# Performance work log

Measured on AMD Instinct MI355X. Metric: run time of the kernel, lower is better.

## Reference

```python
import jax, jax.numpy as jnp
import numpy as np

N_NODES = 200000
N_EVENTS = 100000
MEM_DIM = 100
TIME_DIM = 100
MSG_DIM = 172
T_MAX = 1000000


def setup_inputs() -> dict:
    key = jax.random.key(0)
    ks = jax.random.split(key, 12)
    s = 0.05
    return {
        "memory": jax.random.normal(ks[0], (N_NODES, MEM_DIM), jnp.float32),
        "raw_msg": jax.random.normal(ks[1], (N_EVENTS, MSG_DIM), jnp.float32),
        "time_w": jax.random.normal(ks[2], (TIME_DIM, 1), jnp.float32) * s,
        "time_b": jax.random.normal(ks[3], (TIME_DIM,), jnp.float32) * s,
        "w_ih": jax.random.normal(ks[4], (3 * MEM_DIM, 2 * MEM_DIM + MSG_DIM + TIME_DIM), jnp.float32) * s,
        "w_hh": jax.random.normal(ks[5], (3 * MEM_DIM, MEM_DIM), jnp.float32) * s,
        "b_ih": jax.random.normal(ks[6], (3 * MEM_DIM,), jnp.float32) * s,
        "b_hh": jax.random.normal(ks[7], (3 * MEM_DIM,), jnp.float32) * s,
        "last_update": jax.random.randint(ks[8], (N_NODES,), 0, T_MAX, jnp.int32),
        "src": jax.random.randint(ks[9], (N_EVENTS,), 0, N_NODES, jnp.int32),
        "dst": jax.random.randint(ks[10], (N_EVENTS,), 0, N_NODES, jnp.int32),
        "t": jax.random.randint(ks[11], (N_EVENTS,), 0, T_MAX, jnp.int32),
    }


def _time_enc(t_rel, time_w, time_b):
    # Linear(1, time_dim) followed by cos, as in TGN.update_memory
    return jnp.cos(t_rel[:, None] * time_w[:, 0][None, :] + time_b[None, :])


def _gru_cell(x, h, w_ih, w_hh, b_ih, b_hh):
    gi = x @ w_ih.T + b_ih  # [N, 3*D]
    gh = h @ w_hh.T + b_hh
    i_r, i_z, i_n = jnp.split(gi, 3, axis=-1)
    h_r, h_z, h_n = jnp.split(gh, 3, axis=-1)
    r = jax.nn.sigmoid(i_r + h_r)
    z = jax.nn.sigmoid(i_z + h_z)
    n = jnp.tanh(i_n + r * h_n)
    return (1.0 - z) * n + z * h


def reference(memory, raw_msg, time_w, time_b, w_ih, w_hh, b_ih, b_hh,
              last_update, src, dst, t):
    # time-relative encodings for source- and destination-side messages
    t_rel_s = (t - last_update[src]).astype(memory.dtype)
    t_rel_d = (t - last_update[dst]).astype(memory.dtype)
    t_enc_s = _time_enc(t_rel_s, time_w, time_b)  # [E, time_dim]
    t_enc_d = _time_enc(t_rel_d, time_w, time_b)

    mem_s = memory[src]  # [E, D]
    mem_d = memory[dst]

    # IdentityMessage: concat(mem_self, mem_other, raw_msg, t_enc)
    msg_s = jnp.concatenate([mem_s, mem_d, raw_msg, t_enc_s], axis=-1)  # [E, 472]
    msg_d = jnp.concatenate([mem_d, mem_s, raw_msg, t_enc_d], axis=-1)

    idx = jnp.concatenate([src, dst], axis=0)          # [2E]
    msgs = jnp.concatenate([msg_s, msg_d], axis=0)      # [2E, 472]

    n_nodes = memory.shape[0]
    # MeanAggregator: per-node mean of incoming messages
    summed = jax.ops.segment_sum(msgs, idx, num_segments=n_nodes)  # [N, 472]
    counts = jax.ops.segment_sum(jnp.ones((idx.shape[0],), memory.dtype), idx,
                                 num_segments=n_nodes)             # [N]
    aggr = summed / jnp.maximum(counts, 1.0)[:, None]

    # GRU memory update, applied only to nodes that received messages
    h_new = _gru_cell(aggr, memory, w_ih, w_hh, b_ih, b_hh)
    touched = (counts > 0)[:, None]
    return jnp.where(touched, h_new, memory)  # [N, memory_dim]
```

## Files before the change

kernel.cpp:

```cpp
#include <hip/hip_runtime.h>
#include <math.h>

#define NND 200000
#define NEV 100000
#define MD 100
#define TD 100
#define MSGD 172
#define NB 64
#define NFRAG 25
#define KS 15
#define BP_ELEMS (KS * NFRAG * 64 * 8)
#define GLS 74

typedef __attribute__((ext_vector_type(8))) short bf16x8;
typedef __attribute__((ext_vector_type(4))) float f32x4;

__device__ __forceinline__ float fast_sigmoid(float x) {
    return 1.0f / (1.0f + __expf(-x));
}
__device__ __forceinline__ float fast_tanh(float x) {
    return fmaf(2.0f, 1.0f / (1.0f + __expf(-2.0f * x)), -1.0f);
}

__device__ __forceinline__ unsigned short f2bf(float f) {
    union { float f; unsigned int u; } v; v.f = f;
    unsigned int r = (v.u + 0x7FFFu + ((v.u >> 16) & 1u)) >> 16;
    return (unsigned short)r;
}
__device__ __forceinline__ float bf2f(unsigned int h) {
    union { unsigned int u; float f; } v; v.u = h << 16;
    return v.f;
}
__device__ __forceinline__ unsigned int pk(float a, float b) {
    unsigned int r;
    asm("v_cvt_pk_bf16_f32 %0, %1, %2" : "=v"(r) : "v"(a), "v"(b));
    return r;
}

__global__ __launch_bounds__(256) void k_count(
    const int* __restrict__ src, const int* __restrict__ dst, int* __restrict__ cnt)
{
    int e = blockIdx.x * 256 + threadIdx.x;
    if (e >= NEV) return;
    atomicAdd(&cnt[src[e]], 1);
    atomicAdd(&cnt[dst[e]], 1);
}

__global__ __launch_bounds__(256) void k_scan1(
    const int* __restrict__ cnt, int* __restrict__ off, int* __restrict__ tpos,
    int* __restrict__ psum, int* __restrict__ psumT)
{
    __shared__ int s1[256], s2[256];
    int t = threadIdx.x, b = blockIdx.x;
    int i0 = b * 1024 + t * 4;
    int v0 = (i0 + 0 < NND) ? cnt[i0 + 0] : 0;
    int v1 = (i0 + 1 < NND) ? cnt[i0 + 1] : 0;
    int v2 = (i0 + 2 < NND) ? cnt[i0 + 2] : 0;
    int v3 = (i0 + 3 < NND) ? cnt[i0 + 3] : 0;
    int f0 = v0 > 0, f1 = v1 > 0, f2 = v2 > 0, f3 = v3 > 0;
    int tsum = v0 + v1 + v2 + v3;
    int fsum = f0 + f1 + f2 + f3;
    s1[t] = tsum; s2[t] = fsum;
    __syncthreads();
    for (int o = 1; o < 256; o <<= 1) {
        int x1 = (t >= o) ? s1[t - o] : 0;
        int x2 = (t >= o) ? s2[t - o] : 0;
        __syncthreads();
        s1[t] += x1; s2[t] += x2;
        __syncthreads();
    }
    int e1 = s1[t] - tsum;
    int e2 = s2[t] - fsum;
    if (i0 + 0 < NND) { off[i0 + 0] = e1;                 tpos[i0 + 0] = e2; }
    if (i0 + 1 < NND) { off[i0 + 1] = e1 + v0;            tpos[i0 + 1] = e2 + f0; }
    if (i0 + 2 < NND) { off[i0 + 2] = e1 + v0 + v1;       tpos[i0 + 2] = e2 + f0 + f1; }
    if (i0 + 3 < NND) { off[i0 + 3] = e1 + v0 + v1 + v2;  tpos[i0 + 3] = e2 + f0 + f1 + f2; }
    if (t == 255) { psum[b] = s1[255]; psumT[b] = s2[255]; }
}

__global__ __launch_bounds__(256) void k_scan2(
    int* __restrict__ psum, int* __restrict__ psumT, int* __restrict__ ntp, int nblk)
{
    __shared__ int s1[256], s2[256];
    int t = threadIdx.x;
    int v1 = (t < nblk) ? psum[t] : 0;
    int v2 = (t < nblk) ? psumT[t] : 0;
    s1[t] = v1; s2[t] = v2;
    __syncthreads();
    for (int o = 1; o < 256; o <<= 1) {
        int x1 = (t >= o) ? s1[t - o] : 0;
        int x2 = (t >= o) ? s2[t - o] : 0;
        __syncthreads();
        s1[t] += x1; s2[t] += x2;
        __syncthreads();
    }
    if (t < nblk) { psum[t] = s1[t] - v1; psumT[t] = s2[t] - v2; }
    if (t == nblk - 1) ntp[0] = s2[t];
}

__global__ __launch_bounds__(256) void k_scan3(
    int* __restrict__ off, int* __restrict__ tpos,
    const int* __restrict__ psum, const int* __restrict__ psumT, int* __restrict__ cur)
{
    int t = threadIdx.x, b = blockIdx.x;
    int base = psum[b];
    int baseT = psumT[b];
    int i0 = b * 1024 + t * 4;
#pragma unroll
    for (int j = 0; j < 4; ++j) {
        int i = i0 + j;
        if (i < NND) {
            int v = off[i] + base;
            off[i] = v;
            cur[i] = v;
            tpos[i] += baseT;
        }
    }
}

__global__ __launch_bounds__(256) void k_copytouch(
    const float* __restrict__ memory, const int* __restrict__ cnt,
    const int* __restrict__ off, const int* __restrict__ tpos,
    float* __restrict__ out, int4* __restrict__ tinfo)
{
    int idx = blockIdx.x * 256 + threadIdx.x;
    if (idx >= NND * 25) return;
    int node = idx / 25, u = idx - node * 25;
    int c = cnt[node];
    if (c == 0) {
        reinterpret_cast<float4*>(out)[idx] =
            reinterpret_cast<const float4*>(memory)[idx];
    } else if (u == 0) {
        tinfo[tpos[node]] = make_int4(node, c, off[node], 0);
    }
}

__global__ __launch_bounds__(256) void k_place(
    const int* __restrict__ src, const int* __restrict__ dst,
    const int* __restrict__ tarr, const int* __restrict__ last_update,
    int* __restrict__ cur, int4* __restrict__ entries)
{
    int e = blockIdx.x * 256 + threadIdx.x;
    if (e >= NEV) return;
    int s = src[e], d = dst[e], tt = tarr[e];
    int slot = atomicAdd(&cur[s], 1);
    entries[slot] = make_int4(d, e, __float_as_int((float)(tt - last_update[s])), s);
    slot = atomicAdd(&cur[d], 1);
    entries[slot] = make_int4(s, e, __float_as_int((float)(tt - last_update[d])), d);
}

__global__ __launch_bounds__(256) void k_convert(
    const float* __restrict__ w_ih, const float* __restrict__ w_hh,
    const float* __restrict__ memory, const float* __restrict__ raw_msg,
    unsigned short* __restrict__ Bp, uint4* __restrict__ membf,
    uint4* __restrict__ rawbf)
{
    int idx = blockIdx.x * 256 + threadIdx.x;
    if (idx < BP_ELEMS) {
        int e = idx & 7;
        int lane = (idx >> 3) & 63;
        int t = idx >> 9;
        int nf = t % 25;
        int ks = t / 25;
        int col = nf * 16 + (lane & 15);
        int k = ks * 32 + ((lane >> 4) << 3) + e;
        float v = 0.0f;
        if (col < 200) {
            if (k < 472) v = w_ih[col * 472 + k];
            if (k < 100) v += w_hh[col * 100 + k];
        } else if (col < 300) {
            if (k < 472) v = w_ih[col * 472 + k];
        } else {
            if (k < 100) v = w_hh[(col - 100) * 100 + k];
        }
        Bp[idx] = f2bf(v);
        return;
    }
    int j = idx - BP_ELEMS;
    if (j < NND * 13) {
        int node = j / 13, u = j - node * 13;
        const float4* ms = reinterpret_cast<const float4*>(memory + (size_t)node * MD);
        uint4 o = (uint4){0u, 0u, 0u, 0u};
        if (u < 12) {
            float4 x = ms[2 * u], y = ms[2 * u + 1];
            o.x = pk(x.x, x.y); o.y = pk(x.z, x.w);
            o.z = pk(y.x, y.y); o.w = pk(y.z, y.w);
        } else {
            float4 x = ms[24];
            o.x = pk(x.x, x.y); o.y = pk(x.z, x.w);
        }
        membf[j] = o;
        return;
    }
    j -= NND * 13;
    if (j < NEV * 22) {
        int e = j / 22, r = j - e * 22;
        const float4* rs = reinterpret_cast<const float4*>(raw_msg + (size_t)e * MSGD);
        float4 x = rs[2 * r];
        float4 y = (float4){0.f, 0.f, 0.f, 0.f};
        if (2 * r + 1 < 43) y = rs[2 * r + 1];
        uint4 o;
        o.x = pk(x.x, x.y); o.y = pk(x.z, x.w);
        o.z = pk(y.x, y.y); o.w = pk(y.z, y.w);
        rawbf[j] = o;
    }
}

__global__ __launch_bounds__(512, 4) void tgn_gemm(
    const uint4* __restrict__ membf,
    const uint4* __restrict__ rawbf, const int4* __restrict__ entries,
    const float* __restrict__ time_w, const float* __restrict__ time_b,
    const unsigned short* __restrict__ Bp,
    const float* __restrict__ b_ih, const float* __restrict__ b_hh,
    const int* __restrict__ ntp, const int4* __restrict__ tinfo,
    float* __restrict__ out)
{
    __shared__ __align__(16) unsigned short lds[64 * 480];
    __shared__ int node_s[NB], cnt_s[NB], off_s[NB];
    int tid = threadIdx.x;
    int n0 = blockIdx.x * NB;
    int nt = ntp[0];
    if (n0 >= nt) return;

    if (tid < NB) {
        int slot = n0 + tid;
        if (slot < nt) {
            int4 ti = tinfo[slot];
            node_s[tid] = ti.x; cnt_s[tid] = ti.y; off_s[tid] = ti.z;
        } else {
            node_s[tid] = -1; cnt_s[tid] = 0; off_s[tid] = 0;
        }
    }
    __syncthreads();

    int lane = tid & 63;
    int wv = tid >> 6;

    {
        int u = lane;
        bool lOther = (u >= 13 && u <= 24);
        bool lRaw   = (u >= 25 && u <= 45);
        bool lMix   = (u == 12);
        bool lR46   = (u == 46);
        bool lTenc  = (u >= 47 && u <= 58);
        int offA = lOther ? (16 * u - 200) : (16 * u - 400);

        float tw[8], tb[8];
#pragma unroll
        for (int j = 0; j < 8; ++j) { tw[j] = 0.f; tb[j] = 0.f; }
        if (lTenc) {
            int d0 = 8 * u - 372;
            float4 wa = *reinterpret_cast<const float4*>(time_w + d0);
            float4 wb = *reinterpret_cast<const float4*>(time_w + d0 + 4);
            float4 ba = *reinterpret_cast<const float4*>(time_b + d0);
            float4 bb = *reinterpret_cast<const float4*>(time_b + d0 + 4);
            tw[0] = wa.x; tw[1] = wa.y; tw[2] = wa.z; tw[3] = wa.w;
            tw[4] = wb.x; tw[5] = wb.y; tw[6] = wb.z; tw[7] = wb.w;
            tb[0] = ba.x; tb[1] = ba.y; tb[2] = ba.z; tb[3] = ba.w;
            tb[4] = bb.x; tb[5] = bb.y; tb[6] = bb.z; tb[7] = bb.w;
        } else if (lR46) {
            float4 wa = *reinterpret_cast<const float4*>(time_w);
            float4 ba = *reinterpret_cast<const float4*>(time_b);
            tw[4] = wa.x; tw[5] = wa.y; tw[6] = wa.z; tw[7] = wa.w;
            tb[4] = ba.x; tb[5] = ba.y; tb[6] = ba.z; tb[7] = ba.w;
        }

        const char* membc = reinterpret_cast<const char*>(membf);
        const char* rawbc = reinterpret_cast<const char*>(rawbf);

#pragma unroll
        for (int half = 0; half < 2; ++half) {
            int rb = wv * 8 + half * 4;
            int cc[4], oo[4];
#pragma unroll
            for (int r = 0; r < 4; ++r) { cc[r] = cnt_s[rb + r]; oo[r] = off_s[rb + r]; }
            int4 en[4];
#pragma unroll
            for (int r = 0; r < 4; ++r)
                en[r] = (cc[r] > 0) ? entries[oo[r]] : make_int4(0, 0, 0, 0);
            uint4 mreg[4];
#pragma unroll
            for (int r = 0; r < 4; ++r) {
                int nd = node_s[rb + r];
                mreg[r] = (u < 13 && nd >= 0) ? membf[(size_t)nd * 13 + u]
                                              : (uint4){0u, 0u, 0u, 0u};
            }
            uint2 gA[4], gB[4];
#pragma unroll
            for (int r = 0; r < 4; ++r) {
                gA[r] = (uint2){0u, 0u}; gB[r] = (uint2){0u, 0u};
                if (cc[r] > 0) {
                    if (lOther) {
                        const char* p = membc + (size_t)en[r].x * 208 + offA;
                        gA[r] = *reinterpret_cast<const uint2*>(p);
                        gB[r] = *reinterpret_cast<const uint2*>(p + 8);
                    } else if (lMix) {
                        gB[r] = *reinterpret_cast<const uint2*>(membc + (size_t)en[r].x * 208);
                    } else if (lRaw) {
                        const char* p = rawbc + (size_t)en[r].y * 352 + offA;
                        gA[r] = *reinterpret_cast<const uint2*>(p);
                        gB[r] = *reinterpret_cast<const uint2*>(p + 8);
                    } else if (lR46) {
                        gA[r] = *reinterpret_cast<const uint2*>(rawbc + (size_t)en[r].y * 352 + 336);
                    }
                }
            }
#pragma unroll
            for (int r = 0; r < 4; ++r) {
                int c = cc[r];
                uint4 o;
                if (u < 12) {
                    o = mreg[r];
                } else if (c == 1) {
                    if (lMix) {
                        o.x = mreg[r].x; o.y = mreg[r].y; o.z = gB[r].x; o.w = gB[r].y;
                    } else if (lTenc) {
                        float trel = __int_as_float(en[r].z);
                        o.x = pk(__cosf(fmaf(trel, tw[0], tb[0])), __cosf(fmaf(trel, tw[1], tb[1])));
                        o.y = pk(__cosf(fmaf(trel, tw[2], tb[2])), __cosf(fmaf(trel, tw[3], tb[3])));
                        o.z = pk(__cosf(fmaf(trel, tw[4], tb[4])), __cosf(fmaf(trel, tw[5], tb[5])));
                        o.w = pk(__cosf(fmaf(trel, tw[6], tb[6])), __cosf(fmaf(trel, tw[7], tb[7])));
                    } else if (lR46) {
                        float trel = __int_as_float(en[r].z);
                        o.x = gA[r].x; o.y = gA[r].y;
                        o.z = pk(__cosf(fmaf(trel, tw[4], tb[4])), __cosf(fmaf(trel, tw[5], tb[5])));
                        o.w = pk(__cosf(fmaf(trel, tw[6], tb[6])), __cosf(fmaf(trel, tw[7], tb[7])));
                    } else {
                        o.x = gA[r].x; o.y = gA[r].y; o.z = gB[r].x; o.w = gB[r].y;
                    }
                } else {
                    float a0 = bf2f(gA[r].x & 0xffffu), a1 = bf2f(gA[r].x >> 16);
                    float a2 = bf2f(gA[r].y & 0xffffu), a3 = bf2f(gA[r].y >> 16);
                    float a4 = bf2f(gB[r].x & 0xffffu), a5 = bf2f(gB[r].x >> 16);
                    float a6 = bf2f(gB[r].y & 0xffffu), a7 = bf2f(gB[r].y >> 16);
                    if ((lTenc || lR46) && c > 0) {
                        float trel = __int_as_float(en[r].z);
                        if (lTenc) {
                            a0 = __cosf(fmaf(trel, tw[0], tb[0]));
                            a1 = __cosf(fmaf(trel, tw[1], tb[1]));
                            a2 = __cosf(fmaf(trel, tw[2], tb[2]));
                            a3 = __cosf(fmaf(trel, tw[3], tb[3]));
                        }
                        a4 = __cosf(fmaf(trel, tw[4], tb[4]));
                        a5 = __cosf(fmaf(trel, tw[5], tb[5]));
                        a6 = __cosf(fmaf(trel, tw[6], tb[6]));
                        a7 = __cosf(fmaf(trel, tw[7], tb[7]));
                    }
                    int4 e2 = (c > 1) ? entries[oo[r] + 1] : en[r];
                    for (int i = 1; i < c; ++i) {
                        int4 ecur = e2;
                        if (i + 1 < c) e2 = entries[oo[r] + i + 1];
                        uint2 hA = (uint2){0u, 0u}, hB = (uint2){0u, 0u};
                        if (lOther) {
                            const char* p = membc + (size_t)ecur.x * 208 + offA;
                            hA = *reinterpret_cast<const uint2*>(p);
                            hB = *reinterpret_cast<const uint2*>(p + 8);
                        } else if (lMix) {
                            hB = *reinterpret_cast<const uint2*>(membc + (size_t)ecur.x * 208);
                        } else if (lRaw) {
                            const char* p = rawbc + (size_t)ecur.y * 352 + offA;
                            hA = *reinterpret_cast<const uint2*>(p);
                            hB = *reinterpret_cast<const uint2*>(p + 8);
                        } else if (lR46) {
                            hA = *reinterpret_cast<const uint2*>(rawbc + (size_t)ecur.y * 352 + 336);
                        }
                        a0 += bf2f(hA.x & 0xffffu); a1 += bf2f(hA.x >> 16);
                        a2 += bf2f(hA.y & 0xffffu); a3 += bf2f(hA.y >> 16);
                        a4 += bf2f(hB.x & 0xffffu); a5 += bf2f(hB.x >> 16);
                        a6 += bf2f(hB.y & 0xffffu); a7 += bf2f(hB.y >> 16);
                        if (lTenc || lR46) {
                            float trel = __int_as_float(ecur.z);
                            if (lTenc) {
                                a0 += __cosf(fmaf(trel, tw[0], tb[0]));
                                a1 += __cosf(fmaf(trel, tw[1], tb[1]));
                                a2 += __cosf(fmaf(trel, tw[2], tb[2]));
                                a3 += __cosf(fmaf(trel, tw[3], tb[3]));
                            }
                            a4 += __cosf(fmaf(trel, tw[4], tb[4]));
                            a5 += __cosf(fmaf(trel, tw[5], tb[5]));
                            a6 += __cosf(fmaf(trel, tw[6], tb[6]));
                            a7 += __cosf(fmaf(trel, tw[7], tb[7]));
                        }
                    }
                    float ci = 1.0f / fmaxf((float)c, 1.0f);
                    if (u == 12) {
                        o.x = mreg[r].x; o.y = mreg[r].y;
                    } else {
                        o.x = pk(a0 * ci, a1 * ci); o.y = pk(a2 * ci, a3 * ci);
                    }
                    o.z = pk(a4 * ci, a5 * ci);
                    o.w = pk(a6 * ci, a7 * ci);
                }
                if (u < 60) {
                    int nl = rb + r;
                    int byte = (nl * 960 + 16 * u) ^ ((nl & 7) << 4);
                    *reinterpret_cast<uint4*>(reinterpret_cast<char*>(lds) + byte) = o;
                }
            }
        }
    }
    __syncthreads();

    int l15 = lane & 15;
    int kg8 = (lane >> 4) << 3;
    int f0 = (wv == 0) ? 0 : (4 + 3 * (wv - 1));
    int cw = (wv == 0) ? 4 : 3;

    f32x4 acc[4][4];
#pragma unroll
    for (int g = 0; g < 4; ++g)
#pragma unroll
        for (int i = 0; i < 4; ++i) acc[g][i] = (f32x4){0.f, 0.f, 0.f, 0.f};

    const bf16x8* BpB = reinterpret_cast<const bf16x8*>(Bp);
    const char* ldsc = reinterpret_cast<const char*>(lds);

#pragma unroll
    for (int ks = 0; ks < KS; ++ks) {
        int k0 = ks * 32 + kg8;
        const bf16x8* bp = BpB + ((size_t)(ks * NFRAG + f0)) * 64 + lane;
        bf16x8 b[4];
#pragma unroll
        for (int i = 0; i < 4; ++i)
            if (i < cw) b[i] = bp[i * 64];
#pragma unroll
        for (int g = 0; g < 4; ++g) {
            int r = g * 16 + l15;
            int ab = (r * 960 + 2 * k0) ^ ((r & 7) << 4);
            bf16x8 a = *reinterpret_cast<const bf16x8*>(ldsc + ab);
#pragma unroll
            for (int i = 0; i < 4; ++i)
                if (i < cw)
                    acc[g][i] = __builtin_amdgcn_mfma_f32_16x16x32_bf16(a, b[i], acc[g][i], 0, 0, 0);
        }
    }

    float mv[13];
    {
        const char* membc = reinterpret_cast<const char*>(membf);
#pragma unroll
        for (int t = 0; t < 13; ++t) {
            int idx = tid + t * 512;
            mv[t] = 0.f;
            if (idx < NB * MD) {
                int n = idx / MD, j = idx - n * MD;
                int nd = node_s[n];
                if (nd >= 0) {
                    unsigned short h = *reinterpret_cast<const unsigned short*>(
                        membc + (size_t)nd * 208 + 2 * j);
                    mv[t] = bf2f((unsigned int)h);
                }
            }
        }
    }

    __syncthreads();

    unsigned short* Gl = lds;
    int kq = (lane >> 4) << 2;
#pragma unroll
    for (int i = 0; i < 4; ++i) {
        if (i < cw) {
            int col = (f0 + i) * 16 + l15;
            float bias = (col < 200) ? (b_ih[col] + b_hh[col])
                       : (col < 300) ? b_ih[col] : b_hh[col - 100];
#pragma unroll
            for (int g = 0; g < 4; ++g) {
                int node = g * 16 + kq;
#pragma unroll
                for (int rp = 0; rp < 2; ++rp) {
                    *reinterpret_cast<unsigned int*>(&Gl[col * GLS + node + 2 * rp]) =
                        pk(acc[g][i][2 * rp] + bias, acc[g][i][2 * rp + 1] + bias);
                }
            }
        }
    }
    __syncthreads();

#pragma unroll
    for (int t = 0; t < 13; ++t) {
        int idx = tid + t * 512;
        if (idx < NB * MD) {
            int n = idx / MD, j = idx - n * MD;
            int nd = node_s[n];
            if (nd >= 0) {
                float rp = bf2f((unsigned int)Gl[j * GLS + n]);
                float zp = bf2f((unsigned int)Gl[(100 + j) * GLS + n]);
                float inp = bf2f((unsigned int)Gl[(200 + j) * GLS + n]);
                float hnp = bf2f((unsigned int)Gl[(300 + j) * GLS + n]);
                float r = fast_sigmoid(rp);
                float z = fast_sigmoid(zp);
                float nn = fast_tanh(fmaf(r, hnp, inp));
                float h = (1.0f - z) * nn + z * mv[t];
                out[(size_t)nd * MD + j] = h;
            }
        }
    }
}

extern "C" void kernel_launch(void* const* d_in, const int* in_sizes, int n_in,
                              void* d_out, int out_size, void* d_ws, size_t ws_size,
                              hipStream_t stream)
{
    const float* memory      = (const float*)d_in[0];
    const float* raw_msg     = (const float*)d_in[1];
    const float* time_w      = (const float*)d_in[2];
    const float* time_b      = (const float*)d_in[3];
    const float* w_ih        = (const float*)d_in[4];
    const float* w_hh        = (const float*)d_in[5];
    const float* b_ih        = (const float*)d_in[6];
    const float* b_hh        = (const float*)d_in[7];
    const int*   last_update = (const int*)d_in[8];
    const int*   src         = (const int*)d_in[9];
    const int*   dst         = (const int*)d_in[10];
    const int*   tarr        = (const int*)d_in[11];
    float* out = (float*)d_out;

    int* cnt   = (int*)d_ws;
    int* off   = cnt + NND;
    int* cur   = off + NND;
    int* tpos  = cur + NND;
    int* psum  = tpos + NND;
    int* psumT = psum + 256;
    int* ntp   = psumT + 256;
    int4* entries = (int4*)(ntp + 4);
    int4* tinfo = entries + 2 * NEV;
    uint4* membf = (uint4*)(tinfo + NND);
    uint4* rawbf = membf + (size_t)NND * 13;
    unsigned short* Bp = (unsigned short*)(rawbf + (size_t)NEV * 22);
    size_t need = (size_t)((char*)(Bp + BP_ELEMS) - (char*)d_ws);
    if (ws_size < need) return;

    const int NBLK = (NND + 1023) / 1024;
    const int NTILE = NND / NB;
    const int CVT_TOTAL = BP_ELEMS + NND * 13 + NEV * 22;

    hipMemsetAsync(cnt, 0, NND * sizeof(int), stream);
    k_convert<<<(CVT_TOTAL + 255) / 256, 256, 0, stream>>>(w_ih, w_hh, memory, raw_msg,
                                                           Bp, membf, rawbf);
    k_count<<<(NEV + 255) / 256, 256, 0, stream>>>(src, dst, cnt);
    k_scan1<<<NBLK, 256, 0, stream>>>(cnt, off, tpos, psum, psumT);
    k_scan2<<<1, 256, 0, stream>>>(psum, psumT, ntp, NBLK);
    k_scan3<<<NBLK, 256, 0, stream>>>(off, tpos, psum, psumT, cur);
    k_copytouch<<<(NND * 25 + 255) / 256, 256, 0, stream>>>(memory, cnt, off, tpos, out, tinfo);
    k_place<<<(NEV + 255) / 256, 256, 0, stream>>>(src, dst, tarr, last_update, cur, entries);
    tgn_gemm<<<NTILE, 512, 0, stream>>>(membf, rawbf, entries, time_w, time_b,
                                        Bp, b_ih, b_hh, ntp, tinfo, out);
}
```

Baseline: 257.6 us.

## Sort touched nodes by message-count class and batch multi-message gathers

The scan kernels now bucket touched nodes into four classes by in-degree (1, 2, 3, 4+), so each GEMM tile processes nodes with similar message counts. This is meant to reduce wave divergence in the aggregation loop. The gather loop is restructured so the four rows per half iterate together up to their maximum count, which issues their entry and feature loads in parallel instead of walking each row's message chain serially. In exchange the scan carries five channels instead of two, and the single-message fast path that wrote bf16 values directly is removed.

Result: no change. 256.6 us (-0.4%).

```diff
diff --git a/kernel.cpp b/kernel.cpp
--- a/kernel.cpp
+++ b/kernel.cpp
@@ -48,63 +48,103 @@
 
 __global__ __launch_bounds__(256) void k_scan1(
     const int* __restrict__ cnt, int* __restrict__ off, int* __restrict__ tpos,
-    int* __restrict__ psum, int* __restrict__ psumT)
-{
-    __shared__ int s1[256], s2[256];
+    int* __restrict__ psum, int* __restrict__ psumC)
+{
+    __shared__ int s[5][256];
     int t = threadIdx.x, b = blockIdx.x;
     int i0 = b * 1024 + t * 4;
-    int v0 = (i0 + 0 < NND) ? cnt[i0 + 0] : 0;
-    int v1 = (i0 + 1 < NND) ? cnt[i0 + 1] : 0;
-    int v2 = (i0 + 2 < NND) ? cnt[i0 + 2] : 0;
-    int v3 = (i0 + 3 < NND) ? cnt[i0 + 3] : 0;
-    int f0 = v0 > 0, f1 = v1 > 0, f2 = v2 > 0, f3 = v3 > 0;
-    int tsum = v0 + v1 + v2 + v3;
-    int fsum = f0 + f1 + f2 + f3;
-    s1[t] = tsum; s2[t] = fsum;
+    int v[4], cls[4];
+#pragma unroll
+    for (int j = 0; j < 4; ++j) {
+        v[j] = (i0 + j < NND) ? cnt[i0 + j] : 0;
+        cls[j] = (v[j] == 0) ? -1 : ((v[j] < 4 ? v[j] : 4) - 1);
+    }
+    int tsum = v[0] + v[1] + v[2] + v[3];
+    int fs[4] = {0, 0, 0, 0};
+#pragma unroll
+    for (int j = 0; j < 4; ++j)
+        if (cls[j] >= 0) fs[cls[j]]++;
+    s[0][t] = tsum;
+#pragma unroll
+    for (int X = 0; X < 4; ++X) s[1 + X][t] = fs[X];
     __syncthreads();
     for (int o = 1; o < 256; o <<= 1) {
-        int x1 = (t >= o) ? s1[t - o] : 0;
-        int x2 = (t >= o) ? s2[t - o] : 0;
+        int x[5];
+#pragma unroll
+        for (int ch = 0; ch < 5; ++ch) x[ch] = (t >= o) ? s[ch][t - o] : 0;
         __syncthreads();
-        s1[t] += x1; s2[t] += x2;
+#pragma unroll
+        for (int ch = 0; ch < 5; ++ch) s[ch][t] += x[ch];
         __syncthreads();
     }
-    int e1 = s1[t] - tsum;
-    int e2 = s2[t] - fsum;
-    if (i0 + 0 < NND) { off[i0 + 0] = e1;                 tpos[i0 + 0] = e2; }
-    if (i0 + 1 < NND) { off[i0 + 1] = e1 + v0;            tpos[i0 + 1] = e2 + f0; }
-    if (i0 + 2 < NND) { off[i0 + 2] = e1 + v0 + v1;       tpos[i0 + 2] = e2 + f0 + f1; }
-    if (i0 + 3 < NND) { off[i0 + 3] = e1 + v0 + v1 + v2;  tpos[i0 + 3] = e2 + f0 + f1 + f2; }
-    if (t == 255) { psum[b] = s1[255]; psumT[b] = s2[255]; }
+    int e0 = s[0][t] - tsum;
+    int eC[4];
+#pragma unroll
+    for (int X = 0; X < 4; ++X) eC[X] = s[1 + X][t] - fs[X];
+    int run = 0;
+    int cseen[4] = {0, 0, 0, 0};
+#pragma unroll
+    for (int j = 0; j < 4; ++j) {
+        int i = i0 + j;
+        if (i < NND) {
+            off[i] = e0 + run;
+            if (cls[j] >= 0) tpos[i] = eC[cls[j]] + cseen[cls[j]];
+        }
+        run += v[j];
+        if (cls[j] >= 0) cseen[cls[j]]++;
+    }
+    if (t == 255) {
+        psum[b] = s[0][255];
+#pragma unroll
+        for (int X = 0; X < 4; ++X) psumC[X * 256 + b] = s[1 + X][255];
+    }
 }
 
 __global__ __launch_bounds__(256) void k_scan2(
-    int* __restrict__ psum, int* __restrict__ psumT, int* __restrict__ ntp, int nblk)
-{
-    __shared__ int s1[256], s2[256];
+    int* __restrict__ psum, int* __restrict__ psumC,
+    int* __restrict__ clsBase, int* __restrict__ ntp, int nblk)
+{
+    __shared__ int s[5][256];
     int t = threadIdx.x;
-    int v1 = (t < nblk) ? psum[t] : 0;
-    int v2 = (t < nblk) ? psumT[t] : 0;
-    s1[t] = v1; s2[t] = v2;
+    int v[5];
+    v[0] = (t < nblk) ? psum[t] : 0;
+#pragma unroll
+    for (int X = 0; X < 4; ++X) v[1 + X] = (t < nblk) ? psumC[X * 256 + t] : 0;
+#pragma unroll
+    for (int ch = 0; ch < 5; ++ch) s[ch][t] = v[ch];
     __syncthreads();
     for (int o = 1; o < 256; o <<= 1) {
-        int x1 = (t >= o) ? s1[t - o] : 0;
-        int x2 = (t >= o) ? s2[t - o] : 0;
+        int x[5];
+#pragma unroll
+        for (int ch = 0; ch < 5; ++ch) x[ch] = (t >= o) ? s[ch][t - o] : 0;
         __syncthreads();
-        s1[t] += x1; s2[t] += x2;
+#pragma unroll
+        for (int ch = 0; ch < 5; ++ch) s[ch][t] += x[ch];
         __syncthreads();
     }
-    if (t < nblk) { psum[t] = s1[t] - v1; psumT[t] = s2[t] - v2; }
-    if (t == nblk - 1) ntp[0] = s2[t];
+    if (t < nblk) {
+        psum[t] = s[0][t] - v[0];
+#pragma unroll
+        for (int X = 0; X < 4; ++X) psumC[X * 256 + t] = s[1 + X][t] - v[1 + X];
+    }
+    if (t == 0) {
+        int T0 = s[1][nblk - 1], T1 = s[2][nblk - 1];
+        int T2 = s[3][nblk - 1], T3 = s[4][nblk - 1];
+        clsBase[0] = 0;
+        clsBase[1] = T0;
+        clsBase[2] = T0 + T1;
+        clsBase[3] = T0 + T1 + T2;
+        ntp[0] = T0 + T1 + T2 + T3;
+    }
 }
 
 __global__ __launch_bounds__(256) void k_scan3(
-    int* __restrict__ off, int* __restrict__ tpos,
-    const int* __restrict__ psum, const int* __restrict__ psumT, int* __restrict__ cur)
+    const int* __restrict__ cnt, int* __restrict__ off, int* __restrict__ tpos,
+    const int* __restrict__ psum, const int* __restrict__ psumC,
+    const int* __restrict__ clsBase, int* __restrict__ cur)
 {
     int t = threadIdx.x, b = blockIdx.x;
     int base = psum[b];
-    int baseT = psumT[b];
     int i0 = b * 1024 + t * 4;
 #pragma unroll
     for (int j = 0; j < 4; ++j) {
@@ -113,7 +153,11 @@
             int v = off[i] + base;
             off[i] = v;
             cur[i] = v;
-            tpos[i] += baseT;
+            int c = cnt[i];
+            if (c > 0) {
+                int cls = (c < 4 ? c : 4) - 1;
+                tpos[i] = clsBase[cls] + psumC[cls * 256 + b] + tpos[i];
+            }
         }
     }
 }
@@ -274,6 +318,7 @@
             int cc[4], oo[4];
 #pragma unroll
             for (int r = 0; r < 4; ++r) { cc[r] = cnt_s[rb + r]; oo[r] = off_s[rb + r]; }
+            int maxc = max(max(cc[0], cc[1]), max(cc[2], cc[3]));
             int4 en[4];
 #pragma unroll
             for (int r = 0; r < 4; ++r)
@@ -305,91 +350,88 @@
                     }
                 }
             }
+            float ac[4][8];
 #pragma unroll
             for (int r = 0; r < 4; ++r) {
-                int c = cc[r];
+                ac[r][0] = bf2f(gA[r].x & 0xffffu); ac[r][1] = bf2f(gA[r].x >> 16);
+                ac[r][2] = bf2f(gA[r].y & 0xffffu); ac[r][3] = bf2f(gA[r].y >> 16);
+                ac[r][4] = bf2f(gB[r].x & 0xffffu); ac[r][5] = bf2f(gB[r].x >> 16);
+                ac[r][6] = bf2f(gB[r].y & 0xffffu); ac[r][7] = bf2f(gB[r].y >> 16);
+                if ((lTenc || lR46) && cc[r] > 0) {
+                    float trel = __int_as_float(en[r].z);
+                    if (lTenc) {
+                        ac[r][0] = __cosf(fmaf(trel, tw[0], tb[0]));
+                        ac[r][1] = __cosf(fmaf(trel, tw[1], tb[1]));
+                        ac[r][2] = __cosf(fmaf(trel, tw[2], tb[2]));
+                        ac[r][3] = __cosf(fmaf(trel, tw[3], tb[3]));
+                    }
+                    ac[r][4] = __cosf(fmaf(trel, tw[4], tb[4]));
+                    ac[r][5] = __cosf(fmaf(trel, tw[5], tb[5]));
+                    ac[r][6] = __cosf(fmaf(trel, tw[6], tb[6]));
+                    ac[r][7] = __cosf(fmaf(trel, tw[7], tb[7]));
+                }
+            }
+            for (int j = 1; j < maxc; ++j) {
+                int4 e2[4];
+#pragma unroll
+                for (int r = 0; r < 4; ++r) {
+                    int slot = oo[r] + ((j < cc[r]) ? j : 0);
+                    e2[r] = entries[slot];
+                }
+                uint2 hA[4], hB[4];
+#pragma unroll
+                for (int r = 0; r < 4; ++r) {
+                    hA[r] = (uint2){0u, 0u}; hB[r] = (uint2){0u, 0u};
+                    if (j < cc[r]) {
+                        if (lOther) {
+                            const char* p = membc + (size_t)e2[r].x * 208 + offA;
+                            hA[r] = *reinterpret_cast<const uint2*>(p);
+                            hB[r] = *reinterpret_cast<const uint2*>(p + 8);
+                        } else if (lMix) {
+                            hB[r] = *reinterpret_cast<const uint2*>(membc + (size_t)e2[r].x * 208);
+                        } else if (lRaw) {
+                            const char* p = rawbc + (size_t)e2[r].y * 352 + offA;
+                            hA[r] = *reinterpret_cast<const uint2*>(p);
+                            hB[r] = *reinterpret_cast<const uint2*>(p + 8);
+                        } else if (lR46) {
+                            hA[r] = *reinterpret_cast<const uint2*>(rawbc + (size_t)e2[r].y * 352 + 336);
+                        }
+                    }
+                }
+#pragma unroll
+                for (int r = 0; r < 4; ++r) {
+                    if (j < cc[r]) {
+                        ac[r][0] += bf2f(hA[r].x & 0xffffu); ac[r][1] += bf2f(hA[r].x >> 16);
+                        ac[r][2] += bf2f(hA[r].y & 0xffffu); ac[r][3] += bf2f(hA[r].y >> 16);
+                        ac[r][4] += bf2f(hB[r].x & 0xffffu); ac[r][5] += bf2f(hB[r].x >> 16);
+                        ac[r][6] += bf2f(hB[r].y & 0xffffu); ac[r][7] += bf2f(hB[r].y >> 16);
+                        if (lTenc || lR46) {
+                            float trel = __int_as_float(e2[r].z);
+                            if (lTenc) {
+                                ac[r][0] += __cosf(fmaf(trel, tw[0], tb[0]));
+                                ac[r][1] += __cosf(fmaf(trel, tw[1], tb[1]));
+                                ac[r][2] += __cosf(fmaf(trel, tw[2], tb[2]));
+                                ac[r][3] += __cosf(fmaf(trel, tw[3], tb[3]));
+                            }
+                            ac[r][4] += __cosf(fmaf(trel, tw[4], tb[4]));
+                            ac[r][5] += __cosf(fmaf(trel, tw[5], tb[5]));
+                            ac[r][6] += __cosf(fmaf(trel, tw[6], tb[6]));
+                            ac[r][7] += __cosf(fmaf(trel, tw[7], tb[7]));
+                        }
+                    }
+                }
+            }
+#pragma unroll
+            for (int r = 0; r < 4; ++r) {
+                float ci = 1.0f / fmaxf((float)cc[r], 1.0f);
                 uint4 o;
                 if (u < 12) {
                     o = mreg[r];
-                } else if (c == 1) {
-                    if (lMix) {
-                        o.x = mreg[r].x; o.y = mreg[r].y; o.z = gB[r].x; o.w = gB[r].y;
-                    } else if (lTenc) {
-                        float trel = __int_as_float(en[r].z);
-                        o.x = pk(__cosf(fmaf(trel, tw[0], tb[0])), __cosf(fmaf(trel, tw[1], tb[1])));
-                        o.y = pk(__cosf(fmaf(trel, tw[2], tb[2])), __cosf(fmaf(trel, tw[3], tb[3])));
-                        o.z = pk(__cosf(fmaf(trel, tw[4], tb[4])), __cosf(fmaf(trel, tw[5], tb[5])));
-                        o.w = pk(__cosf(fmaf(trel, tw[6], tb[6])), __cosf(fmaf(trel, tw[7], tb[7])));
-                    } else if (lR46) {
-                        float trel = __int_as_float(en[r].z);
-                        o.x = gA[r].x; o.y = gA[r].y;
-                        o.z = pk(__cosf(fmaf(trel, tw[4], tb[4])), __cosf(fmaf(trel, tw[5], tb[5])));
-                        o.w = pk(__cosf(fmaf(trel, tw[6], tb[6])), __cosf(fmaf(trel, tw[7], tb[7])));
-                    } else {
-                        o.x = gA[r].x; o.y = gA[r].y; o.z = gB[r].x; o.w = gB[r].y;
-                    }
                 } else {
-                    float a0 = bf2f(gA[r].x & 0xffffu), a1 = bf2f(gA[r].x >> 16);
-                    float a2 = bf2f(gA[r].y & 0xffffu), a3 = bf2f(gA[r].y >> 16);
-                    float a4 = bf2f(gB[r].x & 0xffffu), a5 = bf2f(gB[r].x >> 16);
-                    float a6 = bf2f(gB[r].y & 0xffffu), a7 = bf2f(gB[r].y >> 16);
-                    if ((lTenc || lR46) && c > 0) {
-                        float trel = __int_as_float(en[r].z);
-                        if (lTenc) {
-                            a0 = __cosf(fmaf(trel, tw[0], tb[0]));
-                            a1 = __cosf(fmaf(trel, tw[1], tb[1]));
-                            a2 = __cosf(fmaf(trel, tw[2], tb[2]));
-                            a3 = __cosf(fmaf(trel, tw[3], tb[3]));
-                        }
-                        a4 = __cosf(fmaf(trel, tw[4], tb[4]));
-                        a5 = __cosf(fmaf(trel, tw[5], tb[5]));
-                        a6 = __cosf(fmaf(trel, tw[6], tb[6]));
-                        a7 = __cosf(fmaf(trel, tw[7], tb[7]));
-                    }
-                    int4 e2 = (c > 1) ? entries[oo[r] + 1] : en[r];
-                    for (int i = 1; i < c; ++i) {
-                        int4 ecur = e2;
-                        if (i + 1 < c) e2 = entries[oo[r] + i + 1];
-                        uint2 hA = (uint2){0u, 0u}, hB = (uint2){0u, 0u};
-                        if (lOther) {
-                            const char* p = membc + (size_t)ecur.x * 208 + offA;
-                            hA = *reinterpret_cast<const uint2*>(p);
-                            hB = *reinterpret_cast<const uint2*>(p + 8);
-                        } else if (lMix) {
-                            hB = *reinterpret_cast<const uint2*>(membc + (size_t)ecur.x * 208);
-                        } else if (lRaw) {
-                            const char* p = rawbc + (size_t)ecur.y * 352 + offA;
-                            hA = *reinterpret_cast<const uint2*>(p);
-                            hB = *reinterpret_cast<const uint2*>(p + 8);
-                        } else if (lR46) {
-                            hA = *reinterpret_cast<const uint2*>(rawbc + (size_t)ecur.y * 352 + 336);
-                        }
-                        a0 += bf2f(hA.x & 0xffffu); a1 += bf2f(hA.x >> 16);
-                        a2 += bf2f(hA.y & 0xffffu); a3 += bf2f(hA.y >> 16);
-                        a4 += bf2f(hB.x & 0xffffu); a5 += bf2f(hB.x >> 16);
-                        a6 += bf2f(hB.y & 0xffffu); a7 += bf2f(hB.y >> 16);
-                        if (lTenc || lR46) {
-                            float trel = __int_as_float(ecur.z);
-                            if (lTenc) {
-                                a0 += __cosf(fmaf(trel, tw[0], tb[0]));
-                                a1 += __cosf(fmaf(trel, tw[1], tb[1]));
-                                a2 += __cosf(fmaf(trel, tw[2], tb[2]));
-                                a3 += __cosf(fmaf(trel, tw[3], tb[3]));
-                            }
-                            a4 += __cosf(fmaf(trel, tw[4], tb[4]));
-                            a5 += __cosf(fmaf(trel, tw[5], tb[5]));
-                            a6 += __cosf(fmaf(trel, tw[6], tb[6]));
-                            a7 += __cosf(fmaf(trel, tw[7], tb[7]));
-                        }
-                    }
-                    float ci = 1.0f / fmaxf((float)c, 1.0f);
-                    if (u == 12) {
-                        o.x = mreg[r].x; o.y = mreg[r].y;
-                    } else {
-                        o.x = pk(a0 * ci, a1 * ci); o.y = pk(a2 * ci, a3 * ci);
-                    }
-                    o.z = pk(a4 * ci, a5 * ci);
-                    o.w = pk(a6 * ci, a7 * ci);
+                    o.x = (u == 12) ? mreg[r].x : pk(ac[r][0] * ci, ac[r][1] * ci);
+                    o.y = (u == 12) ? mreg[r].y : pk(ac[r][2] * ci, ac[r][3] * ci);
+                    o.z = pk(ac[r][4] * ci, ac[r][5] * ci);
+                    o.w = pk(ac[r][6] * ci, ac[r][7] * ci);
                 }
                 if (u < 60) {
                     int nl = rb + r;
@@ -516,13 +558,14 @@
     const int*   tarr        = (const int*)d_in[11];
     float* out = (float*)d_out;
 
-    int* cnt   = (int*)d_ws;
-    int* off   = cnt + NND;
-    int* cur   = off + NND;
-    int* tpos  = cur + NND;
-    int* psum  = tpos + NND;
-    int* psumT = psum + 256;
-    int* ntp   = psumT + 256;
+    int* cnt     = (int*)d_ws;
+    int* off     = cnt + NND;
+    int* cur     = off + NND;
+    int* tpos    = cur + NND;
+    int* psum    = tpos + NND;
+    int* psumC   = psum + 256;
+    int* clsBase = psumC + 1024;
+    int* ntp     = clsBase + 4;
     int4* entries = (int4*)(ntp + 4);
     int4* tinfo = entries + 2 * NEV;
     uint4* membf = (uint4*)(tinfo + NND);
@@ -539,9 +582,9 @@
     k_convert<<<(CVT_TOTAL + 255) / 256, 256, 0, stream>>>(w_ih, w_hh, memory, raw_msg,
                                                            Bp, membf, rawbf);
     k_count<<<(NEV + 255) / 256, 256, 0, stream>>>(src, dst, cnt);
-    k_scan1<<<NBLK, 256, 0, stream>>>(cnt, off, tpos, psum, psumT);
-    k_scan2<<<1, 256, 0, stream>>>(psum, psumT, ntp, NBLK);
-    k_scan3<<<NBLK, 256, 0, stream>>>(off, tpos, psum, psumT, cur);
+    k_scan1<<<NBLK, 256, 0, stream>>>(cnt, off, tpos, psum, psumC);
+    k_scan2<<<1, 256, 0, stream>>>(psum, psumC, clsBase, ntp, NBLK);
+    k_scan3<<<NBLK, 256, 0, stream>>>(cnt, off, tpos, psum, psumC, clsBase, cur);
     k_copytouch<<<(NND * 25 + 255) / 256, 256, 0, stream>>>(memory, cnt, off, tpos, out, tinfo);
     k_place<<<(NEV + 255) / 256, 256, 0, stream>>>(src, dst, tarr, last_update, cur, entries);
     tgn_gemm<<<NTILE, 512, 0, stream>>>(membf, rawbf, entries, time_w, time_b,
```
